# Kernel tuning notes

Hardware: AMD Instinct MI355X
Metric: run time of the kernel (lower is better)

## Reference

```python
import jax, jax.numpy as jnp
import numpy as np

N_WIRES = 10
DEPTH = 2
BATCH = 16384
DIM = 2 ** N_WIRES
N_ENC = min(N_WIRES, 4)


def _cnot_perm(n, c, t):
    # wire 0 is the most-significant bit (torchquantum convention)
    idx = np.arange(2 ** n)
    ctrl = (idx >> (n - 1 - c)) & 1
    return idx ^ (ctrl << (n - 1 - t))


def _ring_perm(n):
    # composition of CNOT(0,1)...CNOT(n-2,n-1), CNOT(n-1,0) as one basis permutation
    perm = np.arange(2 ** n)
    for w in range(n - 1):
        perm = perm[_cnot_perm(n, w, w + 1)]
    perm = perm[_cnot_perm(n, n - 1, 0)]
    return perm


RING_PERM = jnp.asarray(_ring_perm(N_WIRES))
_idx = np.arange(DIM)
# Z_SIGNS[i, w] = +1 if bit of wire w in basis state i is 0, else -1
Z_SIGNS = jnp.asarray(np.stack(
    [1.0 - 2.0 * ((_idx >> (N_WIRES - 1 - w)) & 1) for w in range(N_WIRES)],
    axis=1).astype(np.float32))  # (DIM, N_WIRES)


def _apply_rx(st, cos_h, sin_h, w):
    # RX(theta) = [[cos(t/2), -i sin(t/2)], [-i sin(t/2), cos(t/2)]] on wire w
    # st: (B, DIM) complex64; cos_h/sin_h: scalar (shared param) or (B,) (encoder)
    b = st.shape[0]
    st = st.reshape(b, 2 ** w, 2, -1)
    a0 = st[:, :, 0, :]
    a1 = st[:, :, 1, :]
    c = jnp.reshape(cos_h, (-1, 1, 1))
    s = jnp.reshape(sin_h, (-1, 1, 1))
    n0 = c * a0 - 1j * s * a1
    n1 = -1j * s * a0 + c * a1
    return jnp.stack([n0, n1], axis=2).reshape(b, -1)


def setup_inputs() -> dict:
    key = jax.random.key(0)
    k1, k2 = jax.random.split(key)
    x = jax.random.normal(k1, (BATCH, N_ENC), dtype=jnp.float32)
    theta = 0.1 * jax.random.normal(k2, (N_WIRES,), dtype=jnp.float32)
    return {"x": x, "theta": theta}


def reference(x, theta):
    b = x.shape[0]
    # |0...0> initial state
    st = jnp.zeros((b, DIM), dtype=jnp.complex64).at[:, 0].set(1.0)
    # encoder: RX(x[:, i]) on wire i
    half = x * 0.5
    for i in range(N_ENC):
        st = _apply_rx(st, jnp.cos(half[:, i]), jnp.sin(half[:, i]), i)
    ct = jnp.cos(theta * 0.5)
    sn = jnp.sin(theta * 0.5)
    for _ in range(DEPTH):
        for w in range(N_WIRES):
            st = _apply_rx(st, ct[w], sn[w], w)
        st = st[:, RING_PERM]  # fused CNOT ring
    probs = jnp.real(st * jnp.conj(st))  # (B, DIM)
    return probs @ Z_SIGNS  # (B, N_WIRES) PauliZ expectations
```

## Files before the change

kernel.cpp:

```cpp
#include <hip/hip_runtime.h>
#include <math.h>

#define BATCH 16384
#define NW 10
#define DEPTH 2


__device__ __forceinline__ void sim_column(int a, int lane,
                                           const float* ct, const float* st_,
                                           float re[16], float im[16])
{
#pragma unroll
    for (int r = 0; r < 16; ++r) { re[r] = 0.0f; im[r] = 0.0f; }
    if (lane == 0) re[a] = 1.0f;

#pragma unroll 1
    for (int d = 0; d < DEPTH; ++d) {
#pragma unroll
        for (int w = 0; w < 4; ++w) {
            const float c = ct[w], s = st_[w];
            const int m = 8 >> w;
#pragma unroll
            for (int r = 0; r < 16; ++r) {
                if (!(r & m)) {
                    const int r1 = r | m;
                    const float a0r = re[r],  a0i = im[r];
                    const float a1r = re[r1], a1i = im[r1];
                    re[r]  = c * a0r + s * a1i;
                    im[r]  = c * a0i - s * a1r;
                    re[r1] = c * a1r + s * a0i;
                    im[r1] = c * a1i - s * a0r;
                }
            }
        }
#pragma unroll
        for (int w = 4; w < 10; ++w) {
            const float c = ct[w], s = st_[w];
            const int lm = 32 >> (w - 4);
#pragma unroll
            for (int r = 0; r < 16; ++r) {
                const float pr = __shfl_xor(re[r], lm, 64);
                const float pi = __shfl_xor(im[r], lm, 64);
                re[r] = c * re[r] + s * pi;
                im[r] = c * im[r] - s * pr;
            }
        }
#pragma unroll
        for (int w = 0; w < 3; ++w) {
            const int cm = 8 >> w, tm = 8 >> (w + 1);
#pragma unroll
            for (int r = 0; r < 16; ++r) {
                if ((r & cm) && !(r & tm)) {
                    const int r2 = r | tm;
                    float t;
                    t = re[r]; re[r] = re[r2]; re[r2] = t;
                    t = im[r]; im[r] = im[r2]; im[r2] = t;
                }
            }
        }
#pragma unroll
        for (int r = 0; r < 16; ++r) {
            if (r & 1) {
                re[r] = __shfl_xor(re[r], 32, 64);
                im[r] = __shfl_xor(im[r], 32, 64);
            }
        }
#pragma unroll
        for (int w = 4; w < 9; ++w) {
            const int cm = 32 >> (w - 4), tm = 32 >> (w - 3);
            const bool ctl = (lane & cm) != 0;
#pragma unroll
            for (int r = 0; r < 16; ++r) {
                const float pr = __shfl_xor(re[r], tm, 64);
                const float pi = __shfl_xor(im[r], tm, 64);
                re[r] = ctl ? pr : re[r];
                im[r] = ctl ? pi : im[r];
            }
        }
        {
            const bool ctl = (lane & 1) != 0;
#pragma unroll
            for (int r = 0; r < 8; ++r) {
                const float t0r = re[r], t1r = re[r + 8];
                const float t0i = im[r], t1i = im[r + 8];
                re[r]     = ctl ? t1r : t0r;
                re[r + 8] = ctl ? t0r : t1r;
                im[r]     = ctl ? t1i : t0i;
                im[r + 8] = ctl ? t0i : t1i;
            }
        }
    }
}

__global__ __launch_bounds__(64) void kA_pairs(const float* __restrict__ theta,
                                               float* __restrict__ Cg)
{
    const int lane = threadIdx.x;

    int t = blockIdx.x, a = 0;
    while (t >= 16 - a) { t -= 16 - a; ++a; }
    const int b = a + t;

    float ct[NW], st_[NW];
#pragma unroll
    for (int w = 0; w < NW; ++w) {
        const float h = 0.5f * theta[w];
        ct[w] = __cosf(h); st_[w] = __sinf(h);
    }

    float ar[16], ai[16], br[16], bi[16];
    sim_column(a, lane, ct, st_, ar, ai);
    if (b == a) {
#pragma unroll
        for (int r = 0; r < 16; ++r) { br[r] = ar[r]; bi[r] = ai[r]; }
    } else {
        sim_column(b, lane, ct, st_, br, bi);
    }

    const int p = (__popc(a) - __popc(b)) & 3;
    const bool odd = (p & 1) != 0;

    float red[10];
#pragma unroll
    for (int k = 0; k < 10; ++k) red[k] = 0.0f;
#pragma unroll
    for (int r = 0; r < 16; ++r) {
        const float vr = ar[r] * br[r] + ai[r] * bi[r];
        const float vi = ar[r] * bi[r] - ai[r] * br[r];
        const float v  = odd ? vi : vr;
        red[0] += (r & 8) ? -v : v;
        red[1] += (r & 4) ? -v : v;
        red[2] += (r & 2) ? -v : v;
        red[3] += (r & 1) ? -v : v;
        red[4] += v;
    }
    const float T = red[4];
    red[4] = (lane & 32) ? -T : T;
    red[5] = (lane & 16) ? -T : T;
    red[6] = (lane &  8) ? -T : T;
    red[7] = (lane &  4) ? -T : T;
    red[8] = (lane &  2) ? -T : T;
    red[9] = (lane &  1) ? -T : T;

#pragma unroll
    for (int k = 0; k < 10; ++k) {
        float v = red[k];
#pragma unroll
        for (int ofs = 32; ofs >= 1; ofs >>= 1)
            v += __shfl_xor(v, ofs, 64);
        red[k] = v;
    }

    if (lane == 0) {
        const float sg = (p == 1 || p == 2) ? -1.0f : 1.0f;
#pragma unroll
        for (int w = 0; w < NW; ++w) {
            const float val = sg * red[w];
            Cg[(a * 16 + b) * 12 + w] = val;
            Cg[(b * 16 + a) * 12 + w] = val;
        }
    }
}

__global__ __launch_bounds__(256) void kB_eval(const float* __restrict__ x,
                                               const float* __restrict__ Cg,
                                               float* __restrict__ out)
{
    __shared__ float sC[256 * 12];
    __shared__ float sK[81 * 12];
    for (int i = threadIdx.x; i < 256 * 12; i += 256) sC[i] = Cg[i];
    __syncthreads();

    for (int idx = threadIdx.x; idx < 810; idx += 256) {
        const int t = idx / 10, w = idx - 10 * t;
        int d0 = t / 27, r0 = t - d0 * 27;
        int d1 = r0 / 9, r1 = r0 - d1 * 9;
        int d2 = r1 / 3, d3 = r1 - d2 * 3;
        const int d[4] = { d0, d1, d2, d3 };

        float s = 0.0f;
#pragma unroll
        for (int e = 0; e < 16; ++e) {
            int aa = 0, bb = 0; float sgn = 1.0f;
#pragma unroll
            for (int qq = 0; qq < 4; ++qq) {
                const int eq = (e >> (3 - qq)) & 1;
                int aq, bq;
                if (d[qq] == 2) { aq = eq; bq = 1 - eq; }
                else {
                    aq = eq; bq = eq;
                    if (d[qq] == 1 && eq) sgn = -sgn;
                }
                aa |= aq << (3 - qq);
                bb |= bq << (3 - qq);
            }
            s += sgn * sC[(aa * 16 + bb) * 12 + w];
        }
        sK[t * 12 + w] = s * 0.0625f;
    }
    __syncthreads();

    const int bidx = blockIdx.x * 256 + threadIdx.x;
    const float4 xv = ((const float4*)x)[bidx];

    float s0, c0, s1, c1, s2, c2, s3, c3;
    __sincosf(xv.x, &s0, &c0);
    __sincosf(xv.y, &s1, &c1);
    __sincosf(xv.z, &s2, &c2);
    __sincosf(xv.w, &s3, &c3);

    const float b0[3] = { 1.0f, c0, s0 };
    const float b1[3] = { 1.0f, c1, s1 };
    const float b2[3] = { 1.0f, c2, s2 };
    const float b3[3] = { 1.0f, c3, s3 };
    float B01[9], B23[9];
#pragma unroll
    for (int i = 0; i < 3; ++i)
#pragma unroll
        for (int j = 0; j < 3; ++j) {
            B01[i * 3 + j] = b0[i] * b1[j];
            B23[i * 3 + j] = b2[i] * b3[j];
        }

    float z[NW];
#pragma unroll
    for (int w = 0; w < NW; ++w) z[w] = 0.0f;

#pragma unroll
    for (int t01 = 0; t01 < 9; ++t01) {
#pragma unroll
        for (int t23 = 0; t23 < 9; ++t23) {
            const float P = B01[t01] * B23[t23];
            const float* base = &sK[(t01 * 9 + t23) * 12];
            const float4 q0 = *(const float4*)(base + 0);
            const float4 q1 = *(const float4*)(base + 4);
            const float4 q2 = *(const float4*)(base + 8);
            z[0] = fmaf(P, q0.x, z[0]);
            z[1] = fmaf(P, q0.y, z[1]);
            z[2] = fmaf(P, q0.z, z[2]);
            z[3] = fmaf(P, q0.w, z[3]);
            z[4] = fmaf(P, q1.x, z[4]);
            z[5] = fmaf(P, q1.y, z[5]);
            z[6] = fmaf(P, q1.z, z[6]);
            z[7] = fmaf(P, q1.w, z[7]);
            z[8] = fmaf(P, q2.x, z[8]);
            z[9] = fmaf(P, q2.y, z[9]);
        }
    }

    float2* po = (float2*)(out + bidx * NW);
    po[0] = make_float2(z[0], z[1]);
    po[1] = make_float2(z[2], z[3]);
    po[2] = make_float2(z[4], z[5]);
    po[3] = make_float2(z[6], z[7]);
    po[4] = make_float2(z[8], z[9]);
}

extern "C" void kernel_launch(void* const* d_in, const int* in_sizes, int n_in,
                              void* d_out, int out_size, void* d_ws, size_t ws_size,
                              hipStream_t stream) {
    const float* x     = (const float*)d_in[0];
    const float* theta = (const float*)d_in[1];
    float* out = (float*)d_out;
    float* Cg  = (float*)d_ws;

    hipLaunchKernelGGL(kA_pairs, dim3(136), dim3(64),  0, stream, theta, Cg);
    hipLaunchKernelGGL(kB_eval,  dim3(BATCH / 256), dim3(256), 0, stream, x, Cg, out);
}
```

Before: 81.96 us.

## Simulate basis columns once and compute pair overlaps inside eval kernel

```diff
diff --git a/kernel.cpp b/kernel.cpp
--- a/kernel.cpp
+++ b/kernel.cpp
@@ -6,13 +6,23 @@
 #define DEPTH 2
 
 
-__device__ __forceinline__ void sim_column(int a, int lane,
-                                           const float* ct, const float* st_,
-                                           float re[16], float im[16])
+__global__ __launch_bounds__(64, 1) void k1_basis(const float* __restrict__ theta,
+                                                  float2* __restrict__ u)
 {
+    const int lane = threadIdx.x;
+    const int a = blockIdx.x;
+
+    float re[16], im[16];
 #pragma unroll
     for (int r = 0; r < 16; ++r) { re[r] = 0.0f; im[r] = 0.0f; }
     if (lane == 0) re[a] = 1.0f;
+
+    float ct[NW], st_[NW];
+#pragma unroll
+    for (int w = 0; w < NW; ++w) {
+        const float h = 0.5f * theta[w];
+        ct[w] = __cosf(h); st_[w] = __sinf(h);
+    }
 
 #pragma unroll 1
     for (int d = 0; d < DEPTH; ++d) {
@@ -90,85 +100,72 @@
             }
         }
     }
+
+#pragma unroll
+    for (int r = 0; r < 16; ++r)
+        u[a * 1024 + (r << 6) + lane] = make_float2(re[r], im[r]);
 }
 
-__global__ __launch_bounds__(64) void kA_pairs(const float* __restrict__ theta,
-                                               float* __restrict__ Cg)
-{
-    const int lane = threadIdx.x;
-
-    int t = blockIdx.x, a = 0;
-    while (t >= 16 - a) { t -= 16 - a; ++a; }
-    const int b = a + t;
-
-    float ct[NW], st_[NW];
-#pragma unroll
-    for (int w = 0; w < NW; ++w) {
-        const float h = 0.5f * theta[w];
-        ct[w] = __cosf(h); st_[w] = __sinf(h);
-    }
-
-    float ar[16], ai[16], br[16], bi[16];
-    sim_column(a, lane, ct, st_, ar, ai);
-    if (b == a) {
-#pragma unroll
-        for (int r = 0; r < 16; ++r) { br[r] = ar[r]; bi[r] = ai[r]; }
-    } else {
-        sim_column(b, lane, ct, st_, br, bi);
-    }
-
-    const int p = (__popc(a) - __popc(b)) & 3;
-    const bool odd = (p & 1) != 0;
-
-    float red[10];
-#pragma unroll
-    for (int k = 0; k < 10; ++k) red[k] = 0.0f;
-#pragma unroll
-    for (int r = 0; r < 16; ++r) {
-        const float vr = ar[r] * br[r] + ai[r] * bi[r];
-        const float vi = ar[r] * bi[r] - ai[r] * br[r];
-        const float v  = odd ? vi : vr;
-        red[0] += (r & 8) ? -v : v;
-        red[1] += (r & 4) ? -v : v;
-        red[2] += (r & 2) ? -v : v;
-        red[3] += (r & 1) ? -v : v;
-        red[4] += v;
-    }
-    const float T = red[4];
-    red[4] = (lane & 32) ? -T : T;
-    red[5] = (lane & 16) ? -T : T;
-    red[6] = (lane &  8) ? -T : T;
-    red[7] = (lane &  4) ? -T : T;
-    red[8] = (lane &  2) ? -T : T;
-    red[9] = (lane &  1) ? -T : T;
-
-#pragma unroll
-    for (int k = 0; k < 10; ++k) {
-        float v = red[k];
-#pragma unroll
-        for (int ofs = 32; ofs >= 1; ofs >>= 1)
-            v += __shfl_xor(v, ofs, 64);
-        red[k] = v;
-    }
-
-    if (lane == 0) {
-        const float sg = (p == 1 || p == 2) ? -1.0f : 1.0f;
-#pragma unroll
-        for (int w = 0; w < NW; ++w) {
-            const float val = sg * red[w];
-            Cg[(a * 16 + b) * 12 + w] = val;
-            Cg[(b * 16 + a) * 12 + w] = val;
-        }
-    }
-}
-
 __global__ __launch_bounds__(256) void kB_eval(const float* __restrict__ x,
-                                               const float* __restrict__ Cg,
+                                               const float2* __restrict__ u,
                                                float* __restrict__ out)
 {
     __shared__ float sC[256 * 12];
     __shared__ float sK[81 * 12];
-    for (int i = threadIdx.x; i < 256 * 12; i += 256) sC[i] = Cg[i];
+
+    const int lane = threadIdx.x & 63;
+    const int wv   = threadIdx.x >> 6;
+
+    for (int p = wv; p < 136; p += 4) {
+        int t = p, a = 0;
+        while (t >= 16 - a) { t -= 16 - a; ++a; }
+        const int b = a + t;
+
+        const int pp = (__popc(a) - __popc(b)) & 3;
+        const bool odd = (pp & 1) != 0;
+
+        float acc0 = 0.0f, acc1 = 0.0f, acc2 = 0.0f, acc3 = 0.0f, accT = 0.0f;
+#pragma unroll
+        for (int r = 0; r < 16; ++r) {
+            const float2 ua = u[a * 1024 + (r << 6) + lane];
+            const float2 ub = u[b * 1024 + (r << 6) + lane];
+            const float vr = ua.x * ub.x + ua.y * ub.y;
+            const float vi = ua.x * ub.y - ua.y * ub.x;
+            const float v  = odd ? vi : vr;
+            acc0 += (r & 8) ? -v : v;
+            acc1 += (r & 4) ? -v : v;
+            acc2 += (r & 2) ? -v : v;
+            acc3 += (r & 1) ? -v : v;
+            accT += v;
+        }
+        float red[10];
+        red[0] = acc0; red[1] = acc1; red[2] = acc2; red[3] = acc3;
+        red[4] = (lane & 32) ? -accT : accT;
+        red[5] = (lane & 16) ? -accT : accT;
+        red[6] = (lane &  8) ? -accT : accT;
+        red[7] = (lane &  4) ? -accT : accT;
+        red[8] = (lane &  2) ? -accT : accT;
+        red[9] = (lane &  1) ? -accT : accT;
+
+#pragma unroll
+        for (int k = 0; k < 10; ++k) {
+            float v = red[k];
+#pragma unroll
+            for (int ofs = 32; ofs >= 1; ofs >>= 1)
+                v += __shfl_xor(v, ofs, 64);
+            red[k] = v;
+        }
+
+        if (lane == 0) {
+            const float sg = (pp == 1 || pp == 2) ? -1.0f : 1.0f;
+#pragma unroll
+            for (int w = 0; w < NW; ++w) {
+                const float val = sg * red[w];
+                sC[(a * 16 + b) * 12 + w] = val;
+                sC[(b * 16 + a) * 12 + w] = val;
+            }
+        }
+    }
     __syncthreads();
 
     for (int idx = threadIdx.x; idx < 810; idx += 256) {
@@ -262,8 +259,8 @@
     const float* x     = (const float*)d_in[0];
     const float* theta = (const float*)d_in[1];
     float* out = (float*)d_out;
-    float* Cg  = (float*)d_ws;
-
-    hipLaunchKernelGGL(kA_pairs, dim3(136), dim3(64),  0, stream, theta, Cg);
-    hipLaunchKernelGGL(kB_eval,  dim3(BATCH / 256), dim3(256), 0, stream, x, Cg, out);
+    float2* u  = (float2*)d_ws;
+
+    hipLaunchKernelGGL(k1_basis, dim3(16), dim3(64),  0, stream, theta, u);
+    hipLaunchKernelGGL(kB_eval,  dim3(BATCH / 256), dim3(256), 0, stream, x, u, out);
 }
```

After: 128.4 us. +56.7%, slower.
